# Kernel optimization log

Hardware: AMD Instinct MI355X
Metric: run time of the kernel (lower is better)

The kernel has to match this reference:

```python
import jax, jax.numpy as jnp
import numpy as np

NUM_HEADS = 12

def setup_inputs() -> dict:
    key = jax.random.key(0)
    ks = jax.random.split(key, 6)
    B, N, C = 16, 1024, 768
    H, d = NUM_HEADS, C // NUM_HEADS
    return {
        "x": jax.random.normal(ks[0], (B, N, C), dtype=jnp.float32),
        "W_qkv": jax.random.normal(ks[1], (C, 3 * C), dtype=jnp.float32) * 0.02,
        "b_qkv": jax.random.normal(ks[2], (3 * C,), dtype=jnp.float32) * 0.02,
        "zeta": jnp.ones((1, 1, H, 1, d), dtype=jnp.float32),
        "W_proj": jax.random.normal(ks[3], (C, C), dtype=jnp.float32) * 0.02,
        "b_proj": jax.random.normal(ks[4], (C,), dtype=jnp.float32) * 0.02,
        "mask": jnp.zeros((B, N), dtype=bool),
    }

def reference(x, W_qkv, b_qkv, zeta, W_proj, b_proj, mask):
    B, N, C = x.shape
    H = NUM_HEADS
    d = C // H
    scale = d ** -0.5
    # qkv: (B,N,3C) -> (B,N,3,H,d) -> (3,B,H,N,d), gated by zeta (1,1,H,1,d)
    qkv = (x @ W_qkv + b_qkv).reshape(B, N, 3, H, d).transpose(2, 0, 3, 1, 4)
    qkv = qkv * zeta
    q, k, v = qkv[0], qkv[1], qkv[2]
    attn = jnp.einsum("bhnd,bhmd->bhnm", q, k) * scale
    # mask (B,N) over keys -> (B,1,1,N)
    attn = jnp.where(mask[:, None, None, :], -jnp.inf, attn)
    attn = jax.nn.softmax(attn, axis=-1)
    out = jnp.einsum("bhnm,bhmd->bhnd", attn, v)          # (B,H,N,d)
    out = out.transpose(0, 2, 1, 3).reshape(B, N, C)
    return out @ W_proj + b_proj
```

## Files before the change

### kernel.cpp

```cpp
#include <hip/hip_runtime.h>
#include <hip/hip_bf16.h>

typedef unsigned short ushort_t;
typedef __bf16 bf16_t;
typedef bf16_t bf16x8 __attribute__((ext_vector_type(8)));
typedef float floatx4 __attribute__((ext_vector_type(4)));
typedef ushort_t ushortx8 __attribute__((ext_vector_type(8)));

struct alignas(8) us4 { ushort_t x, y, z, w; };

__device__ __forceinline__ ushort_t f2bf(float f) {
  union { float f; unsigned int u; } v; v.f = f;
  unsigned int u = v.u;
  return (ushort_t)((u + 0x7fffu + ((u >> 16) & 1u)) >> 16);
}

__device__ __forceinline__ unsigned int pk_bf16(float a, float b) {
  __hip_bfloat162 h = __float22bfloat162_rn(float2{a, b});
  union { __hip_bfloat162 h; unsigned int u; } v; v.h = h;
  return v.u;
}

__device__ __forceinline__ void async16(const void* g, void* l) {
  __builtin_amdgcn_global_load_lds(
      (const __attribute__((address_space(1))) unsigned int*)g,
      (__attribute__((address_space(3))) unsigned int*)l, 16, 0, 0);
}

#define LOG2E 1.44269504088896340736f


__global__ __launch_bounds__(256) void k_prep(const float* __restrict__ x,
                                              ushort_t* __restrict__ xb,
                                              const float* __restrict__ Wq,
                                              ushort_t* __restrict__ WqT,
                                              const float* __restrict__ Wp,
                                              ushort_t* __restrict__ WpT) {
  __shared__ float tile[32][33];
  const int bid = blockIdx.x, t = threadIdx.x;
  if (bid < 6144) {
    size_t i = ((size_t)bid * 256 + t) * 8;
    float4 a = *(const float4*)(x + i);
    float4 b = *(const float4*)(x + i + 4);
    ushortx8 o;
    o[0] = f2bf(a.x); o[1] = f2bf(a.y); o[2] = f2bf(a.z); o[3] = f2bf(a.w);
    o[4] = f2bf(b.x); o[5] = f2bf(b.y); o[6] = f2bf(b.z); o[7] = f2bf(b.w);
    *(ushortx8*)(xb + i) = o;
    return;
  }
  const float* in; ushort_t* out; int C, c0, r0;
  if (bid < 7872) {
    int b2 = bid - 6144;
    in = Wq; out = WqT; C = 2304;
    c0 = (b2 % 72) * 32; r0 = (b2 / 72) * 32;
  } else {
    int b3 = bid - 7872;
    in = Wp; out = WpT; C = 768;
    c0 = (b3 % 24) * 32; r0 = (b3 / 24) * 32;
  }
  const int tx = t & 31, ty = t >> 5;
#pragma unroll
  for (int i = 0; i < 32; i += 8)
    tile[ty + i][tx] = in[(size_t)(r0 + ty + i) * C + c0 + tx];
  __syncthreads();
#pragma unroll
  for (int i = 0; i < 32; i += 8)
    out[(size_t)(c0 + ty + i) * 768 + r0 + tx] = f2bf(tile[tx][ty + i]);
}


template <bool SWAP>
__device__ __forceinline__ void gemm256(const ushort_t* __restrict__ A,
                                        const ushort_t* __restrict__ Bt,
                                        int m0, int n0,
                                        ushort_t* sA, ushort_t* sB,
                                        floatx4 acc[8][4]) {
  const int t = threadIdx.x;
  const int lane = t & 63;
  const int lr = lane & 15, qd = lane >> 4;
  const int w = t >> 6;
  const int wr = w >> 2, wc = w & 3;
  const int swz = ((t & 3) ^ ((t >> 3) & 3)) * 8;
  const ushort_t* gA = A + (size_t)(m0 + (t >> 2)) * 768 + swz;
  const ushort_t* gB = Bt + (size_t)(n0 + (t >> 2)) * 768 + swz;
  char* lA = (char*)sA + t * 16;
  char* lB = (char*)sB + t * 16;
  const int rsz = (qd ^ ((lr >> 1) & 3)) * 16;
#define ISSUE(kk, buf)                                    \
  do {                                                    \
    const int k0_ = (kk) * 32, b_ = (buf) * 16384;        \
    async16(gA + k0_, lA + b_);                           \
    async16(gA + k0_ + 128 * 768, lA + b_ + 8192);        \
    async16(gB + k0_, lB + b_);                           \
    async16(gB + k0_ + 128 * 768, lB + b_ + 8192);        \
  } while (0)
  ISSUE(0, 0);
  asm volatile("s_waitcnt vmcnt(0)" ::: "memory");
  asm volatile("s_barrier" ::: "memory");
#pragma unroll
  for (int k = 0; k < 24; ++k) {
    if (k + 1 < 24) ISSUE(k + 1, (k + 1) & 1);
    const char* cA = (const char*)sA + (k & 1) * 16384;
    const char* cB = (const char*)sB + (k & 1) * 16384;
    bf16x8 af[8], bfr[4];
#pragma unroll
    for (int i = 0; i < 8; ++i)
      af[i] = *(const bf16x8*)(cA + (wr * 128 + i * 16 + lr) * 64 + rsz);
#pragma unroll
    for (int j = 0; j < 4; ++j)
      bfr[j] = *(const bf16x8*)(cB + (wc * 64 + j * 16 + lr) * 64 + rsz);
#pragma unroll
    for (int i = 0; i < 8; ++i)
#pragma unroll
      for (int j = 0; j < 4; ++j) {
        if constexpr (SWAP)
          acc[i][j] = __builtin_amdgcn_mfma_f32_16x16x32_bf16(bfr[j], af[i], acc[i][j], 0, 0, 0);
        else
          acc[i][j] = __builtin_amdgcn_mfma_f32_16x16x32_bf16(af[i], bfr[j], acc[i][j], 0, 0, 0);
      }
    if (k + 1 < 24) {
      asm volatile("s_waitcnt vmcnt(0)" ::: "memory");
      asm volatile("s_barrier" ::: "memory");
    }
  }
#undef ISSUE
}


__global__ __launch_bounds__(512, 2) void k_qkv(const ushort_t* __restrict__ xb,
                                                const ushort_t* __restrict__ WqT,
                                                const float* __restrict__ bqkv,
                                                const float* __restrict__ zeta,
                                                ushort_t* __restrict__ qb,
                                                ushort_t* __restrict__ kb,
                                                ushort_t* __restrict__ vtb) {
  __shared__ alignas(16) ushort_t sA[2 * 8192];
  __shared__ alignas(16) ushort_t sB[2 * 8192];
  floatx4 acc[8][4] = {};
  const int lin = blockIdx.x;
  const int xcd = lin & 7, idx = lin >> 3;
  const int m0 = (xcd * 8 + (idx & 7)) * 256;
  const int n0 = (idx >> 3) * 256;
  const int tq = n0 / 768;
  const int t = threadIdx.x, lane = t & 63, w = t >> 6;
  const int wr = w >> 2, wc = w & 3, lr = lane & 15, qd = lane >> 4;
  if (tq < 2) {
    gemm256<true>(xb, WqT, m0, n0, sA, sB, acc);
    ushort_t* dst = (tq == 0) ? qb : kb;
    const float sc = (tq == 0) ? 0.125f * LOG2E : 1.0f;
#pragma unroll
    for (int j = 0; j < 4; ++j) {
      int n = n0 + wc * 64 + j * 16 + qd * 4;
      int nc = n - tq * 768;
      int h = nc >> 6, dim = nc & 63;
      float4 b4 = *(const float4*)&bqkv[n];
      float4 z4 = *(const float4*)&zeta[nc];
      float g0 = z4.x * sc, g1 = z4.y * sc, g2 = z4.z * sc, g3 = z4.w * sc;
#pragma unroll
      for (int i = 0; i < 8; ++i) {
        int m = m0 + wr * 128 + i * 16 + lr;
        int b = m >> 10, seq = m & 1023;
        us4 pk;
        pk.x = f2bf((acc[i][j][0] + b4.x) * g0);
        pk.y = f2bf((acc[i][j][1] + b4.y) * g1);
        pk.z = f2bf((acc[i][j][2] + b4.z) * g2);
        pk.w = f2bf((acc[i][j][3] + b4.w) * g3);
        *(us4*)&dst[(((size_t)b * 12 + h) * 1024 + seq) * 64 + dim] = pk;
      }
    }
  } else {
    gemm256<false>(xb, WqT, m0, n0, sA, sB, acc);
#pragma unroll
    for (int j = 0; j < 4; ++j) {
      int n = n0 + wc * 64 + j * 16 + lr;
      int nc = n - 2 * 768;
      int h = nc >> 6, dim = nc & 63;
      float bias = bqkv[n];
      float zv = zeta[nc];
#pragma unroll
      for (int i = 0; i < 8; ++i) {
        int mbase = m0 + wr * 128 + i * 16 + qd * 4;
        int b = mbase >> 10, seq = mbase & 1023;
        us4 pk;
        pk.x = f2bf((acc[i][j][0] + bias) * zv);
        pk.y = f2bf((acc[i][j][1] + bias) * zv);
        pk.z = f2bf((acc[i][j][2] + bias) * zv);
        pk.w = f2bf((acc[i][j][3] + bias) * zv);
        *(us4*)&vtb[(((size_t)b * 12 + h) * 64 + dim) * 1024 + seq] = pk;
      }
    }
  }
}


template <bool SWAP>
__device__ __forceinline__ void gemm_pipe3(const ushort_t* __restrict__ A,
                                           const ushort_t* __restrict__ Bt,
                                           int m0, int n0,
                                           ushort_t* sA, ushort_t* sB,
                                           floatx4 acc[4][4]) {
  const int t = threadIdx.x;
  const int lane = t & 63;
  const int lr = lane & 15, qd = lane >> 4;
  const int w = t >> 6;
  const int wr = w >> 1, wc = w & 1;
  const int swz = ((t & 3) ^ ((t >> 3) & 3)) * 8;
  const ushort_t* gA = A + (size_t)(m0 + (t >> 2)) * 768 + swz;
  const ushort_t* gB = Bt + (size_t)(n0 + (t >> 2)) * 768 + swz;
  char* lA = (char*)sA + t * 16;
  char* lB = (char*)sB + t * 16;
  const int rsz = (qd ^ ((lr >> 1) & 3)) * 16;
#define ISSUE(kk, buf)                                    \
  do {                                                    \
    const int k0_ = (kk) * 32, b_ = (buf) * 8192;         \
    async16(gA + k0_, lA + b_);                           \
    async16(gA + k0_ + 64 * 768, lA + b_ + 4096);         \
    async16(gB + k0_, lB + b_);                           \
    async16(gB + k0_ + 64 * 768, lB + b_ + 4096);         \
  } while (0)
  ISSUE(0, 0);
  ISSUE(1, 1);
  asm volatile("s_waitcnt vmcnt(4)" ::: "memory");
  asm volatile("s_barrier" ::: "memory");
#pragma unroll
  for (int k = 0; k < 24; ++k) {
    if (k + 2 < 24) ISSUE(k + 2, (k + 2) % 3);
    const char* cA = (const char*)sA + (k % 3) * 8192;
    const char* cB = (const char*)sB + (k % 3) * 8192;
    bf16x8 af[4], bfr[4];
#pragma unroll
    for (int i = 0; i < 4; ++i)
      af[i] = *(const bf16x8*)(cA + (wr * 64 + i * 16 + lr) * 64 + rsz);
#pragma unroll
    for (int j = 0; j < 4; ++j)
      bfr[j] = *(const bf16x8*)(cB + (wc * 64 + j * 16 + lr) * 64 + rsz);
#pragma unroll
    for (int i = 0; i < 4; ++i)
#pragma unroll
      for (int j = 0; j < 4; ++j) {
        if constexpr (SWAP)
          acc[i][j] = __builtin_amdgcn_mfma_f32_16x16x32_bf16(bfr[j], af[i], acc[i][j], 0, 0, 0);
        else
          acc[i][j] = __builtin_amdgcn_mfma_f32_16x16x32_bf16(af[i], bfr[j], acc[i][j], 0, 0, 0);
      }
    if (k < 22)
      asm volatile("s_waitcnt vmcnt(4)" ::: "memory");
    else if (k == 22)
      asm volatile("s_waitcnt vmcnt(0)" ::: "memory");
    if (k < 23) asm volatile("s_barrier" ::: "memory");
  }
#undef ISSUE
}


__global__ __launch_bounds__(256, 3) void k_attn(const ushort_t* __restrict__ qg,
                                                 const ushort_t* __restrict__ kg,
                                                 const ushort_t* __restrict__ vg,
                                                 const unsigned char* __restrict__ mask,
                                                 ushort_t* __restrict__ ob) {
  __shared__ alignas(16) char smem[53248];
  float* maskadd = (float*)(smem + 49152);
  const int t = threadIdx.x, lane = t & 63, w = t >> 6;
  const int lr = lane & 15, qd = lane >> 4;
  const int lin = blockIdx.x;
  const int bh = (lin & 7) + 8 * (lin >> 6);
  const int qt = (lin >> 3) & 7;
  const int b = bh / 12, h = bh % 12;
  const int qrow0 = qt * 128 + w * 32;
  const ushort_t* qp = qg + (size_t)bh * 65536;
  const ushort_t* kp = kg + (size_t)bh * 65536;
  const ushort_t* vp = vg + (size_t)bh * 65536;
  const unsigned char* mp = mask + b * 1024;

  bf16x8 qf[2][2];
#pragma unroll
  for (int ns = 0; ns < 2; ++ns)
#pragma unroll
    for (int kk = 0; kk < 2; ++kk)
      qf[ns][kk] = *(const bf16x8*)(qp + (size_t)(qrow0 + ns * 16 + lr) * 64 + kk * 32 + qd * 8);

  floatx4 o[4][2] = {};
  float lst[2] = {0.f, 0.f};
  char* sPw = smem + 32768 + w * 4096;

  {
    uchar4 mv = *(const uchar4*)(mp + t * 4);
    float4 f;
    f.x = mv.x ? -1e30f : 0.0f;
    f.y = mv.y ? -1e30f : 0.0f;
    f.z = mv.z ? -1e30f : 0.0f;
    f.w = mv.w ? -1e30f : 0.0f;
    *(float4*)&maskadd[t * 4] = f;
  }

#define STAGE_K(kt_, st_)                                                 \
  do {                                                                    \
    const ushort_t* kpt_ = kp + (kt_) * 4096;                             \
    _Pragma("unroll")                                                     \
    for (int it = 0; it < 2; ++it) {                                      \
      int p = it * 256 + t;                                               \
      int r = p >> 3, cs = (p & 7) ^ (r & 7);                             \
      async16(kpt_ + r * 64 + cs * 8, smem + (st_) * 16384 + p * 16);     \
    }                                                                     \
  } while (0)
#define STAGE_V(kt_, st_)                                                 \
  do {                                                                    \
    const ushort_t* vpt_ = vp + (kt_) * 64;                               \
    _Pragma("unroll")                                                     \
    for (int it = 0; it < 2; ++it) {                                      \
      int p = it * 256 + t;                                               \
      int r = p >> 3, cs = (p & 7) ^ (r & 7);                             \
      async16(vpt_ + (size_t)r * 1024 + cs * 8,                           \
              smem + (st_) * 16384 + 8192 + p * 16);                      \
    }                                                                     \
  } while (0)

  STAGE_K(0, 0);
  STAGE_V(0, 0);
  __syncthreads();

#pragma unroll 2
  for (int kt = 0; kt < 16; ++kt) {
    const int st = kt & 1;
    if (kt + 1 < 16) {
      STAGE_K(kt + 1, st ^ 1);
      STAGE_V(kt + 1, st ^ 1);
    }
    const char* sK = smem + st * 16384;
    const char* sV = smem + st * 16384 + 8192;

    floatx4 s[4][2] = {};
    __builtin_amdgcn_s_setprio(1);
#pragma unroll
    for (int kk = 0; kk < 2; ++kk) {
#pragma unroll
      for (int ms = 0; ms < 4; ++ms) {
        bf16x8 ak = *(const bf16x8*)(sK + (ms * 16 + lr) * 128 +
                                     ((kk * 4 + qd) ^ (lr & 7)) * 16);
#pragma unroll
        for (int ns = 0; ns < 2; ++ns)
          s[ms][ns] = __builtin_amdgcn_mfma_f32_16x16x32_bf16(ak, qf[ns][kk], s[ms][ns], 0, 0, 0);
      }
    }
    __builtin_amdgcn_s_setprio(0);

#pragma unroll
    for (int ms = 0; ms < 4; ++ms) {
      float4 mk = *(const float4*)&maskadd[kt * 64 + ms * 16 + qd * 4];
#pragma unroll
      for (int ns = 0; ns < 2; ++ns) {
        float p0 = __builtin_amdgcn_exp2f(s[ms][ns][0] + mk.x);
        float p1 = __builtin_amdgcn_exp2f(s[ms][ns][1] + mk.y);
        float p2 = __builtin_amdgcn_exp2f(s[ms][ns][2] + mk.z);
        float p3 = __builtin_amdgcn_exp2f(s[ms][ns][3] + mk.w);
        lst[ns] += (p0 + p1) + (p2 + p3);
        uint2 pk;
        pk.x = pk_bf16(p0, p1);
        pk.y = pk_bf16(p2, p3);
        *(uint2*)(sPw + (ns * 16 + lr) * 128 +
                  ((ms * 2 + (qd >> 1)) ^ (lr & 7)) * 16 + (qd & 1) * 8) = pk;
      }
    }
    asm volatile("s_waitcnt lgkmcnt(0)" ::: "memory");
    __builtin_amdgcn_sched_barrier(0);

    if (kt + 1 < 16)
      asm volatile("s_waitcnt vmcnt(4)" ::: "memory");
    else
      asm volatile("s_waitcnt vmcnt(0)" ::: "memory");
    asm volatile("s_barrier" ::: "memory");

    __builtin_amdgcn_s_setprio(1);
#pragma unroll
    for (int kk = 0; kk < 2; ++kk) {
      bf16x8 pb[2];
#pragma unroll
      for (int ns = 0; ns < 2; ++ns)
        pb[ns] = *(const bf16x8*)(sPw + (ns * 16 + lr) * 128 +
                                  ((kk * 4 + qd) ^ (lr & 7)) * 16);
#pragma unroll
      for (int ds = 0; ds < 4; ++ds) {
        bf16x8 av = *(const bf16x8*)(sV + (ds * 16 + lr) * 128 +
                                     ((kk * 4 + qd) ^ (lr & 7)) * 16);
#pragma unroll
        for (int ns = 0; ns < 2; ++ns)
          o[ds][ns] = __builtin_amdgcn_mfma_f32_16x16x32_bf16(av, pb[ns], o[ds][ns], 0, 0, 0);
      }
    }
    __builtin_amdgcn_s_setprio(0);

    if (kt + 1 < 16) {
      asm volatile("s_waitcnt vmcnt(2)" ::: "memory");
      asm volatile("s_barrier" ::: "memory");
    }
  }
#undef STAGE_K
#undef STAGE_V

#pragma unroll
  for (int ns = 0; ns < 2; ++ns) {
    lst[ns] += __shfl_xor(lst[ns], 16);
    lst[ns] += __shfl_xor(lst[ns], 32);
  }
#pragma unroll
  for (int ns = 0; ns < 2; ++ns) {
    float rl = 1.0f / lst[ns];
    size_t row = (size_t)(b * 1024 + qrow0 + ns * 16 + lr) * 768 + h * 64;
#pragma unroll
    for (int ds = 0; ds < 4; ++ds) {
      uint2 ov;
      ov.x = pk_bf16(o[ds][ns][0] * rl, o[ds][ns][1] * rl);
      ov.y = pk_bf16(o[ds][ns][2] * rl, o[ds][ns][3] * rl);
      *(uint2*)&ob[row + ds * 16 + qd * 4] = ov;
    }
  }
}


__global__ __launch_bounds__(256, 3) void k_proj(const ushort_t* __restrict__ ob,
                                                 const ushort_t* __restrict__ WpT,
                                                 const float* __restrict__ bproj,
                                                 float* __restrict__ out) {
  __shared__ alignas(16) ushort_t sA[3 * 4096];
  __shared__ alignas(16) ushort_t sB[3 * 4096];
  floatx4 acc[4][4] = {};
  const int lin = blockIdx.x;
  const int xcd = lin & 7, idx = lin >> 3;
  const int m0 = (xcd * 16 + (idx & 15)) * 128;
  const int n0 = (idx >> 4) * 128;
  gemm_pipe3<true>(ob, WpT, m0, n0, sA, sB, acc);
  const int t = threadIdx.x, lane = t & 63, w = t >> 6;
  const int wr = w >> 1, wc = w & 1, lr = lane & 15, qd = lane >> 4;
#pragma unroll
  for (int j = 0; j < 4; ++j) {
    int n = n0 + wc * 64 + j * 16 + qd * 4;
    float4 b4 = *(const float4*)&bproj[n];
#pragma unroll
    for (int i = 0; i < 4; ++i) {
      int m = m0 + wr * 64 + i * 16 + lr;
      float4 o;
      o.x = acc[i][j][0] + b4.x;
      o.y = acc[i][j][1] + b4.y;
      o.z = acc[i][j][2] + b4.z;
      o.w = acc[i][j][3] + b4.w;
      *(float4*)&out[(size_t)m * 768 + n] = o;
    }
  }
}


extern "C" void kernel_launch(void* const* d_in, const int* in_sizes, int n_in,
                              void* d_out, int out_size, void* d_ws, size_t ws_size,
                              hipStream_t stream) {
  const float* x = (const float*)d_in[0];
  const float* bqkv = (const float*)d_in[2];
  const float* zeta = (const float*)d_in[3];
  const float* bproj = (const float*)d_in[5];
  const unsigned char* mask = (const unsigned char*)d_in[6];
  float* out = (float*)d_out;
  char* ws = (char*)d_ws;
  ushort_t* xb  = (ushort_t*)(ws);
  ushort_t* WqT = (ushort_t*)(ws + 25165824);
  ushort_t* WpT = (ushort_t*)(ws + 28704768);
  ushort_t* qb  = (ushort_t*)(ws + 29884416);
  ushort_t* kb  = (ushort_t*)(ws + 55050240);
  ushort_t* vtb = (ushort_t*)(ws + 80216064);
  ushort_t* ob  = xb;

  k_prep<<<dim3(8448), dim3(256), 0, stream>>>(x, xb, (const float*)d_in[1], WqT,
                                               (const float*)d_in[4], WpT);
  k_qkv<<<dim3(576), dim3(512), 0, stream>>>(xb, WqT, bqkv, zeta, qb, kb, vtb);
  k_attn<<<dim3(1536), dim3(256), 0, stream>>>(qb, kb, vtb, mask, ob);
  k_proj<<<dim3(768), dim3(256), 0, stream>>>(ob, WpT, bproj, out);
}
```

Measured before the change: 303.0 us.

## Deepen QKV GEMM pipeline to four LDS stages with split-phase MFMA scheduling

Replaces the QKV GEMM's double-buffered LDS pipeline with a four-stage ring held in 128 KB of dynamic shared memory, prefetching three k-steps ahead. Each k-step is split into two halves, with A and B tile loads interleaved between them. MFMA bursts are wrapped in setprio and sched_barrier so memory latency overlaps with matrix math instead of stalling at a full vmcnt(0) every step. The cost is that each 512-thread block now needs 128 KB of LDS, so only one block fits per CU instead of two, and the 576-block grid needs more waves.

Result: no change. 307.8 us (+1.6%).

```diff
diff --git a/kernel.cpp b/kernel.cpp
--- a/kernel.cpp
+++ b/kernel.cpp
@@ -70,11 +70,11 @@
 
 
 template <bool SWAP>
-__device__ __forceinline__ void gemm256(const ushort_t* __restrict__ A,
-                                        const ushort_t* __restrict__ Bt,
-                                        int m0, int n0,
-                                        ushort_t* sA, ushort_t* sB,
-                                        floatx4 acc[8][4]) {
+__device__ __forceinline__ void gemm256_8ph(const ushort_t* __restrict__ A,
+                                            const ushort_t* __restrict__ Bt,
+                                            int m0, int n0,
+                                            char* smem,
+                                            floatx4 acc[8][4]) {
   const int t = threadIdx.x;
   const int lane = t & 63;
   const int lr = lane & 15, qd = lane >> 4;
@@ -83,34 +83,44 @@
   const int swz = ((t & 3) ^ ((t >> 3) & 3)) * 8;
   const ushort_t* gA = A + (size_t)(m0 + (t >> 2)) * 768 + swz;
   const ushort_t* gB = Bt + (size_t)(n0 + (t >> 2)) * 768 + swz;
-  char* lA = (char*)sA + t * 16;
-  char* lB = (char*)sB + t * 16;
+  char* lA = smem + t * 16;
+  char* lB = smem + 65536 + t * 16;
   const int rsz = (qd ^ ((lr >> 1) & 3)) * 16;
-#define ISSUE(kk, buf)                                    \
+#define ISSUE_A(kk)                                       \
   do {                                                    \
-    const int k0_ = (kk) * 32, b_ = (buf) * 16384;        \
-    async16(gA + k0_, lA + b_);                           \
-    async16(gA + k0_ + 128 * 768, lA + b_ + 8192);        \
-    async16(gB + k0_, lB + b_);                           \
-    async16(gB + k0_ + 128 * 768, lB + b_ + 8192);        \
+    const int k0_ = (kk) * 32, s_ = ((kk) & 3) * 16384;   \
+    async16(gA + k0_, lA + s_);                           \
+    async16(gA + k0_ + 128 * 768, lA + s_ + 8192);        \
   } while (0)
-  ISSUE(0, 0);
-  asm volatile("s_waitcnt vmcnt(0)" ::: "memory");
+#define ISSUE_B(kk)                                       \
+  do {                                                    \
+    const int k0_ = (kk) * 32, s_ = ((kk) & 3) * 16384;   \
+    async16(gB + k0_, lB + s_);                           \
+    async16(gB + k0_ + 128 * 768, lB + s_ + 8192);        \
+  } while (0)
+  ISSUE_A(0); ISSUE_B(0);
+  ISSUE_A(1); ISSUE_B(1);
+  ISSUE_A(2); ISSUE_B(2);
+  asm volatile("s_waitcnt vmcnt(8)" ::: "memory");
   asm volatile("s_barrier" ::: "memory");
 #pragma unroll
   for (int k = 0; k < 24; ++k) {
-    if (k + 1 < 24) ISSUE(k + 1, (k + 1) & 1);
-    const char* cA = (const char*)sA + (k & 1) * 16384;
-    const char* cB = (const char*)sB + (k & 1) * 16384;
+    const char* cA = smem + (k & 3) * 16384;
+    const char* cB = smem + 65536 + (k & 3) * 16384;
     bf16x8 af[8], bfr[4];
 #pragma unroll
-    for (int i = 0; i < 8; ++i)
+    for (int i = 0; i < 4; ++i)
       af[i] = *(const bf16x8*)(cA + (wr * 128 + i * 16 + lr) * 64 + rsz);
 #pragma unroll
     for (int j = 0; j < 4; ++j)
       bfr[j] = *(const bf16x8*)(cB + (wc * 64 + j * 16 + lr) * 64 + rsz);
-#pragma unroll
-    for (int i = 0; i < 8; ++i)
+    if (k + 3 < 24) ISSUE_A(k + 3);
+    asm volatile("s_barrier" ::: "memory");
+    asm volatile("s_waitcnt lgkmcnt(0)" ::: "memory");
+    __builtin_amdgcn_sched_barrier(0);
+    __builtin_amdgcn_s_setprio(1);
+#pragma unroll
+    for (int i = 0; i < 4; ++i)
 #pragma unroll
       for (int j = 0; j < 4; ++j) {
         if constexpr (SWAP)
@@ -118,12 +128,36 @@
         else
           acc[i][j] = __builtin_amdgcn_mfma_f32_16x16x32_bf16(af[i], bfr[j], acc[i][j], 0, 0, 0);
       }
-    if (k + 1 < 24) {
+    __builtin_amdgcn_s_setprio(0);
+    asm volatile("s_barrier" ::: "memory");
+#pragma unroll
+    for (int i = 4; i < 8; ++i)
+      af[i] = *(const bf16x8*)(cA + (wr * 128 + i * 16 + lr) * 64 + rsz);
+    if (k + 3 < 24) ISSUE_B(k + 3);
+    asm volatile("s_barrier" ::: "memory");
+    asm volatile("s_waitcnt lgkmcnt(0)" ::: "memory");
+    __builtin_amdgcn_sched_barrier(0);
+    __builtin_amdgcn_s_setprio(1);
+#pragma unroll
+    for (int i = 4; i < 8; ++i)
+#pragma unroll
+      for (int j = 0; j < 4; ++j) {
+        if constexpr (SWAP)
+          acc[i][j] = __builtin_amdgcn_mfma_f32_16x16x32_bf16(bfr[j], af[i], acc[i][j], 0, 0, 0);
+        else
+          acc[i][j] = __builtin_amdgcn_mfma_f32_16x16x32_bf16(af[i], bfr[j], acc[i][j], 0, 0, 0);
+      }
+    __builtin_amdgcn_s_setprio(0);
+    if (k <= 20)
+      asm volatile("s_waitcnt vmcnt(8)" ::: "memory");
+    else if (k == 21)
+      asm volatile("s_waitcnt vmcnt(4)" ::: "memory");
+    else if (k == 22)
       asm volatile("s_waitcnt vmcnt(0)" ::: "memory");
-      asm volatile("s_barrier" ::: "memory");
-    }
-  }
-#undef ISSUE
+    if (k < 23) asm volatile("s_barrier" ::: "memory");
+  }
+#undef ISSUE_A
+#undef ISSUE_B
 }
 
 
@@ -134,8 +168,7 @@
                                                 ushort_t* __restrict__ qb,
                                                 ushort_t* __restrict__ kb,
                                                 ushort_t* __restrict__ vtb) {
-  __shared__ alignas(16) ushort_t sA[2 * 8192];
-  __shared__ alignas(16) ushort_t sB[2 * 8192];
+  extern __shared__ char smem[];
   floatx4 acc[8][4] = {};
   const int lin = blockIdx.x;
   const int xcd = lin & 7, idx = lin >> 3;
@@ -145,7 +178,7 @@
   const int t = threadIdx.x, lane = t & 63, w = t >> 6;
   const int wr = w >> 2, wc = w & 3, lr = lane & 15, qd = lane >> 4;
   if (tq < 2) {
-    gemm256<true>(xb, WqT, m0, n0, sA, sB, acc);
+    gemm256_8ph<true>(xb, WqT, m0, n0, smem, acc);
     ushort_t* dst = (tq == 0) ? qb : kb;
     const float sc = (tq == 0) ? 0.125f * LOG2E : 1.0f;
 #pragma unroll
@@ -169,7 +202,7 @@
       }
     }
   } else {
-    gemm256<false>(xb, WqT, m0, n0, sA, sB, acc);
+    gemm256_8ph<false>(xb, WqT, m0, n0, smem, acc);
 #pragma unroll
     for (int j = 0; j < 4; ++j) {
       int n = n0 + wc * 64 + j * 16 + lr;
@@ -467,9 +500,16 @@
   ushort_t* vtb = (ushort_t*)(ws + 80216064);
   ushort_t* ob  = xb;
 
+  static int attr_done = 0;
+  if (!attr_done) {
+    hipFuncSetAttribute(reinterpret_cast<const void*>(&k_qkv),
+                        hipFuncAttributeMaxDynamicSharedMemorySize, 131072);
+    attr_done = 1;
+  }
+
   k_prep<<<dim3(8448), dim3(256), 0, stream>>>(x, xb, (const float*)d_in[1], WqT,
                                                (const float*)d_in[4], WpT);
-  k_qkv<<<dim3(576), dim3(512), 0, stream>>>(xb, WqT, bqkv, zeta, qb, kb, vtb);
+  k_qkv<<<dim3(576), dim3(512), 131072, stream>>>(xb, WqT, bqkv, zeta, qb, kb, vtb);
   k_attn<<<dim3(1536), dim3(256), 0, stream>>>(qb, kb, vtb, mask, ob);
   k_proj<<<dim3(768), dim3(256), 0, stream>>>(ob, WpT, bproj, out);
 }
```
